# Kernel optimization log

Hardware: AMD Instinct MI355X
Metric: run time of the kernel (lower is better)

The kernel has to match this reference:

```python
import jax, jax.numpy as jnp
import numpy as np

N_HEAD, D_MODEL, D_HEAD = 16, 1024, 64
BSZ, SEQ = 4, 2048
SCALE = 1.0 / D_HEAD ** 0.5
LN_EPS = 1e-5
NEG = -1e10


def layer_norm(x, gamma, beta):
    mu = jnp.mean(x, axis=-1, keepdims=True)
    var = jnp.var(x, axis=-1, keepdims=True)
    return (x - mu) * jax.lax.rsqrt(var + LN_EPS) * gamma + beta


def setup_inputs() -> dict:
    key = jax.random.key(0)
    ks = jax.random.split(key, 8)
    q = jax.random.normal(ks[0], (BSZ, SEQ, D_MODEL), dtype=jnp.float32)
    attn_mask = jax.random.randint(ks[1], (SEQ, SEQ), 0, 2).astype(bool)
    s = 1.0 / np.sqrt(D_MODEL)
    Wq = jax.random.normal(ks[2], (D_MODEL, N_HEAD * D_HEAD), dtype=jnp.float32) * s
    Wk = jax.random.normal(ks[3], (D_MODEL, N_HEAD * D_HEAD), dtype=jnp.float32) * s
    Wv = jax.random.normal(ks[4], (D_MODEL, N_HEAD * D_HEAD), dtype=jnp.float32) * s
    Wo = jax.random.normal(ks[5], (N_HEAD * D_HEAD, D_MODEL), dtype=jnp.float32) * s
    gamma = jnp.ones((D_MODEL,), dtype=jnp.float32)
    beta = jnp.zeros((D_MODEL,), dtype=jnp.float32)
    return {"q": q, "attn_mask": attn_mask, "Wq": Wq, "Wk": Wk, "Wv": Wv,
            "Wo": Wo, "gamma": gamma, "beta": beta}


def reference(q, attn_mask, Wq, Wk, Wv, Wo, gamma, beta):
    # pre_lnorm: residual uses the normalized q (as in the torch code, q is reassigned)
    qn = layer_norm(q, gamma, beta)                      # (b, n1, d_model)
    hq = (qn @ Wq).reshape(BSZ, SEQ, N_HEAD, D_HEAD)     # self-attn: k = v = q
    hk = (qn @ Wk).reshape(BSZ, SEQ, N_HEAD, D_HEAD)
    hv = (qn @ Wv).reshape(BSZ, SEQ, N_HEAD, D_HEAD)
    score = jnp.einsum('bind,bjnd->ijbn', hq, hk) * SCALE  # (n1, n2, b, h)
    score = jnp.where(attn_mask[:, :, None, None], NEG, score)
    prob = jax.nn.softmax(score, axis=1)
    vec = jnp.einsum('ijbn,bjnd->bind', prob, hv).reshape(BSZ, SEQ, N_HEAD * D_HEAD)
    attn_out = vec @ Wo
    return qn + attn_out
```

## Files before the change

### kernel.cpp

```cpp
#include <hip/hip_runtime.h>

typedef __bf16 bf16;
typedef __bf16 bf16x8 __attribute__((ext_vector_type(8)));
typedef __bf16 bf16x4 __attribute__((ext_vector_type(4)));
typedef float  f32x4  __attribute__((ext_vector_type(4)));

#define MFMA16 __builtin_amdgcn_mfma_f32_16x16x32_bf16

static constexpr int   BSZ   = 4;
static constexpr int   SEQL  = 2048;
static constexpr int   DM    = 1024;
static constexpr int   NHEAD = 16;
static constexpr int   DHEAD = 64;
static constexpr float SCL2  = 0.125f * 1.44269504f;

__device__ __forceinline__ void glds16(bf16* lds, const bf16* g) {
    __builtin_amdgcn_global_load_lds(
        (const __attribute__((address_space(1))) unsigned int*)g,
        (__attribute__((address_space(3))) unsigned int*)lds, 16, 0, 0);
}

__global__ void detect_mask(const unsigned int* __restrict__ m, int* __restrict__ flag) {
    __shared__ int ok[4];
    if (threadIdx.x < 4) ok[threadIdx.x] = 1;
    __syncthreads();
    for (int i = 0; i < 16; ++i) {
        unsigned int w = m[threadIdx.x * 16 + i];
        if (!(w == 0u || w == 1u)) ok[0] = 0;
        if (w & 0xFEFEFEFEu) ok[1] = 0;
        if (!(w == 0u || w == 0x3F800000u)) ok[2] = 0;
        unsigned lo = w & 0xFFFFu, hi = w >> 16;
        if (!((lo == 0u || lo == 0x3F80u) && (hi == 0u || hi == 0x3F80u))) ok[3] = 0;
    }
    __syncthreads();
    if (threadIdx.x == 0)
        *flag = ok[0] ? 0 : (ok[1] ? 1 : (ok[2] ? 2 : 3));
}

__device__ __forceinline__ bool mask_at(const void* m, int fl, long idx) {
    if (fl == 0) return ((const int*)m)[idx] != 0;
    if (fl == 1) return ((const unsigned char*)m)[idx] != 0;
    if (fl == 2) return ((const float*)m)[idx] != 0.0f;
    return ((const unsigned short*)m)[idx] != 0;
}

__global__ __launch_bounds__(256) void prep_bits(const void* __restrict__ mask,
                                                 const int* __restrict__ flagp,
                                                 unsigned long long* __restrict__ rb) {
    const int fl = *flagp;
    const int word = blockIdx.x * 4 + (threadIdx.x >> 6);
    const long base = (long)word * 64 + (threadIdx.x & 63);
    unsigned long long b = __ballot(mask_at(mask, fl, base));
    if ((threadIdx.x & 63) == 0) rb[word] = b;
}

__global__ __launch_bounds__(256) void prep_words(
    const unsigned long long* __restrict__ rb, unsigned long long* __restrict__ wm)
{
    const int t = threadIdx.x, L = t & 63, w = t >> 6;
    const int pair = blockIdx.x * 4 + w;
    const int qgrp = pair >> 5, kt = pair & 31;
    const unsigned long long r0 = rb[(size_t)(qgrp * 16 + (L & 15)) * 32 + kt];
    const int lq = L >> 4;
    unsigned long long myw = 0;
    #pragma unroll
    for (int jr = 0; jr < 16; ++jr) {
        const int jj = jr >> 2, r = jr & 3;
        const int bitpos = (jj & 1) * 32 + lq * 8 + (jj >> 1) * 4 + r;
        unsigned long long bal = __ballot(((r0 >> bitpos) & 1ull) != 0ull);
        if (L == jr) myw = bal;
    }
    if (L < 16) wm[(size_t)pair * 16 + L] = myw;
}

__global__ __launch_bounds__(256) void ln_kernel(
    const float* __restrict__ x, const float* __restrict__ g,
    const float* __restrict__ bta, bf16* __restrict__ y)
{
    const int row = blockIdx.x, t = threadIdx.x;
    const float4 v = ((const float4*)(x + (size_t)row * DM))[t];
    float s  = v.x + v.y + v.z + v.w;
    float ss = v.x * v.x + v.y * v.y + v.z * v.z + v.w * v.w;
    for (int m = 32; m >= 1; m >>= 1) { s += __shfl_xor(s, m); ss += __shfl_xor(ss, m); }
    __shared__ float red[8];
    const int w = t >> 6, L = t & 63;
    if (L == 0) { red[w] = s; red[4 + w] = ss; }
    __syncthreads();
    s  = red[0] + red[1] + red[2] + red[3];
    ss = red[4] + red[5] + red[6] + red[7];
    const float mu = s * (1.0f / DM);
    const float var = ss * (1.0f / DM) - mu * mu;
    const float r = rsqrtf(var + 1e-5f);
    const float4 gv = ((const float4*)g)[t];
    const float4 bv = ((const float4*)bta)[t];
    bf16x4 o;
    o[0] = (bf16)((v.x - mu) * r * gv.x + bv.x);
    o[1] = (bf16)((v.y - mu) * r * gv.y + bv.y);
    o[2] = (bf16)((v.z - mu) * r * gv.z + bv.z);
    o[3] = (bf16)((v.w - mu) * r * gv.w + bv.w);
    ((bf16x4*)(y + (size_t)row * DM))[t] = o;
}

__global__ void cvt_w(const float* __restrict__ Wq, const float* __restrict__ Wk,
                      const float* __restrict__ Wv, const float* __restrict__ Wo,
                      bf16* __restrict__ Wt)
{
    __shared__ float tile[32][33];
    const int z = blockIdx.z;
    const float* src = (z == 0) ? Wq : (z == 1) ? Wk : (z == 2) ? Wv : Wo;
    const float scl = (z == 1) ? SCL2 : 1.0f;
    bf16* dst = Wt + (size_t)z * DM * DM;
    const int tx = threadIdx.x, ty = threadIdx.y;
    const int nIn = blockIdx.x * 32 + tx;
    const int kIn = blockIdx.y * 32;
    for (int i = 0; i < 32; i += 8)
        tile[ty + i][tx] = src[(size_t)(kIn + ty + i) * DM + nIn];
    __syncthreads();
    const int nOut = blockIdx.x * 32;
    const int kOut = blockIdx.y * 32 + tx;
    for (int i = 0; i < 32; i += 8)
        dst[(size_t)(nOut + ty + i) * DM + kOut] = (bf16)(tile[tx][ty + i] * scl);
}

__device__ __forceinline__ void gemm128_core(
    const bf16* __restrict__ A, const bf16* __restrict__ Bt,
    int m0, int n0, bool swapped, f32x4 acc[4][4], bf16* Asm, bf16* Bsm)
{
    const int t = threadIdx.x, w = t >> 6, L = t & 63;
    const int lr = L & 15, lq = L >> 4;
    const int wm = w & 1, wn = w >> 1;
    const int srow = L >> 3;
    const int scol = ((L & 7) ^ (L >> 3)) * 8;
    const bf16* Ab = A  + (size_t)(m0 + w * 32 + srow) * DM + scol;
    const bf16* Bb = Bt + (size_t)(n0 + w * 32 + srow) * DM + scol;
    bf16* AsmW = Asm + (w * 32) * 64;
    bf16* BsmW = Bsm + (w * 32) * 64;
    for (int kk = 0; kk < DM; kk += 64) {
        __syncthreads();
        glds16(AsmW,           Ab + kk);
        glds16(AsmW +  8 * 64, Ab + (size_t) 8 * DM + kk);
        glds16(AsmW + 16 * 64, Ab + (size_t)16 * DM + kk);
        glds16(AsmW + 24 * 64, Ab + (size_t)24 * DM + kk);
        glds16(BsmW,           Bb + kk);
        glds16(BsmW +  8 * 64, Bb + (size_t) 8 * DM + kk);
        glds16(BsmW + 16 * 64, Bb + (size_t)16 * DM + kk);
        glds16(BsmW + 24 * 64, Bb + (size_t)24 * DM + kk);
        __syncthreads();
        #pragma unroll
        for (int ks = 0; ks < 2; ++ks) {
            bf16x8 af[4], bf_[4];
            #pragma unroll
            for (int i = 0; i < 4; ++i) {
                const int ra = wm * 64 + i * 16 + lr;
                af[i] = *(const bf16x8*)(Asm + ra * 64 + ((((ks << 2) | lq) ^ (lr & 7)) << 3));
            }
            #pragma unroll
            for (int j = 0; j < 4; ++j) {
                const int rb2 = wn * 64 + j * 16 + lr;
                bf_[j] = *(const bf16x8*)(Bsm + rb2 * 64 + ((((ks << 2) | lq) ^ (lr & 7)) << 3));
            }
            if (!swapped) {
                #pragma unroll
                for (int i = 0; i < 4; ++i)
                    #pragma unroll
                    for (int j = 0; j < 4; ++j)
                        acc[i][j] = MFMA16(af[i], bf_[j], acc[i][j], 0, 0, 0);
            } else {
                #pragma unroll
                for (int i = 0; i < 4; ++i)
                    #pragma unroll
                    for (int j = 0; j < 4; ++j)
                        acc[i][j] = MFMA16(bf_[j], af[i], acc[i][j], 0, 0, 0);
            }
        }
    }
}

__global__ __launch_bounds__(256) void qkv128(
    const bf16* __restrict__ qn, const bf16* __restrict__ Wt,
    bf16* __restrict__ Qb, bf16* __restrict__ Kb, bf16* __restrict__ Vtb)
{
    __shared__ __align__(16) bf16 Asm[128 * 64];
    __shared__ __align__(16) bf16 Bsm[128 * 64];
    const int ny = blockIdx.y;
    const int z = ny >> 3;
    const int m0 = blockIdx.x * 128, n0 = (ny & 7) * 128;
    f32x4 acc[4][4] = {};
    gemm128_core(qn, Wt + (size_t)z * DM * DM, m0, n0, z == 2, acc, Asm, Bsm);
    const int t = threadIdx.x, L = t & 63, w = t >> 6;
    const int wm = w & 1, wn = w >> 1, lr = L & 15, lq = L >> 4;
    if (z < 2) {
        bf16* dst = z ? Kb : Qb;
        #pragma unroll
        for (int i = 0; i < 4; ++i)
            #pragma unroll
            for (int j = 0; j < 4; ++j)
                #pragma unroll
                for (int r = 0; r < 4; ++r) {
                    int m = m0 + wm * 64 + i * 16 + lq * 4 + r;
                    int n = n0 + wn * 64 + j * 16 + lr;
                    int b = m >> 11, s = m & 2047, h = n >> 6, d = n & 63;
                    dst[(((size_t)b * NHEAD + h) * SEQL + s) * DHEAD + d] = (bf16)acc[i][j][r];
                }
    } else {
        #pragma unroll
        for (int i = 0; i < 4; ++i)
            #pragma unroll
            for (int j = 0; j < 4; ++j)
                #pragma unroll
                for (int r = 0; r < 4; ++r) {
                    int dg = n0 + wn * 64 + j * 16 + lq * 4 + r;
                    int sg = m0 + wm * 64 + i * 16 + lr;
                    int h = dg >> 6, d = dg & 63, b = sg >> 11, s = sg & 2047;
                    Vtb[(((size_t)b * NHEAD + h) * DHEAD + d) * SEQL + s] = (bf16)acc[i][j][r];
                }
    }
}

__global__ __launch_bounds__(256) void out128(
    const bf16* __restrict__ vec, const bf16* __restrict__ Wot,
    const bf16* __restrict__ qnb, float* __restrict__ out)
{
    __shared__ __align__(16) bf16 Asm[128 * 64];
    __shared__ __align__(16) bf16 Bsm[128 * 64];
    const int m0 = blockIdx.x * 128, n0 = blockIdx.y * 128;
    f32x4 acc[4][4] = {};
    gemm128_core(vec, Wot, m0, n0, false, acc, Asm, Bsm);
    const int t = threadIdx.x, L = t & 63, w = t >> 6;
    const int wm = w & 1, wn = w >> 1, lr = L & 15, lq = L >> 4;
    #pragma unroll
    for (int i = 0; i < 4; ++i)
        #pragma unroll
        for (int j = 0; j < 4; ++j)
            #pragma unroll
            for (int r = 0; r < 4; ++r) {
                int m = m0 + wm * 64 + i * 16 + lq * 4 + r;
                int n = n0 + wn * 64 + j * 16 + lr;
                size_t idx = (size_t)m * DM + n;
                out[idx] = acc[i][j][r] + (float)qnb[idx];
            }
}

__global__ __launch_bounds__(256) void flash_attn(
    const bf16* __restrict__ Qb, const bf16* __restrict__ Kb,
    const bf16* __restrict__ Vtb, const unsigned long long* __restrict__ mb,
    bf16* __restrict__ vec)
{
    __shared__ __align__(16) bf16 Ksm [2][64 * 72];
    __shared__ __align__(16) bf16 Vtsm[2][64 * 72];

    const int t = threadIdx.x, w = t >> 6, L = t & 63;
    const int lr = L & 15, lq = L >> 4;
    const int bid = blockIdx.x;
    const int slot = bid & 7, rest = bid >> 3;
    const int qblk = rest & 15;
    const int bh = ((rest >> 4) << 3) + slot;
    const int b = bh >> 4, h = bh & 15;
    const int q0 = qblk * 128 + w * 32;

    const bf16* Qh  = Qb  + (size_t)bh * SEQL * DHEAD;
    const bf16* Kh  = Kb  + (size_t)bh * SEQL * DHEAD;
    const bf16* Vth = Vtb + (size_t)bh * DHEAD * SEQL;

    bf16x8 qf[2][2];
    #pragma unroll
    for (int qg = 0; qg < 2; ++qg)
        #pragma unroll
        for (int ks = 0; ks < 2; ++ks)
            qf[qg][ks] = *(const bf16x8*)(Qh + (size_t)(q0 + qg * 16 + lr) * DHEAD + ks * 32 + lq * 8);

    const int qgrp0 = __builtin_amdgcn_readfirstlane(q0 >> 4);
    const unsigned long long* wm0 = mb + (size_t)qgrp0 * 512;
    const unsigned long long* wm1 = wm0 + 512;

    f32x4 o[4][2] = {};
    f32x4 lacc[2] = {};

    const bf16 one = (bf16)1.0f;
    const bf16x8 ones8 = {one, one, one, one, one, one, one, one};
    const float fz = 0.0f;

    const int sr = t >> 2, sc = (t & 3) * 16;
    const int zrow = ((sr >> 2) & 1) * 32 + ((sr >> 5) & 1) * 16 + ((sr >> 3) & 3) * 4 + (sr & 3);
    constexpr int NT = SEQL / 64;
    bf16x8 kreg[2], vreg[2];

    kreg[0] = *(const bf16x8*)(Kh  + (size_t)sr * DHEAD + sc);
    kreg[1] = *(const bf16x8*)(Kh  + (size_t)sr * DHEAD + sc + 8);
    vreg[0] = *(const bf16x8*)(Vth + (size_t)sr * SEQL + sc);
    vreg[1] = *(const bf16x8*)(Vth + (size_t)sr * SEQL + sc + 8);
    *(bf16x8*)(Ksm[0]  + zrow * 72 + sc)     = kreg[0];
    *(bf16x8*)(Ksm[0]  + zrow * 72 + sc + 8) = kreg[1];
    *(bf16x8*)(Vtsm[0] + sr * 72 + sc)       = vreg[0];
    *(bf16x8*)(Vtsm[0] + sr * 72 + sc + 8)   = vreg[1];
    kreg[0] = *(const bf16x8*)(Kh  + (size_t)(64 + sr) * DHEAD + sc);
    kreg[1] = *(const bf16x8*)(Kh  + (size_t)(64 + sr) * DHEAD + sc + 8);
    vreg[0] = *(const bf16x8*)(Vth + (size_t)sr * SEQL + 64 + sc);
    vreg[1] = *(const bf16x8*)(Vth + (size_t)sr * SEQL + 64 + sc + 8);
    __syncthreads();

    for (int kt = 0; kt < NT; ++kt) {
        const int cur = kt & 1;
        const bf16* Kc = Ksm[cur];
        const bf16* Vc = Vtsm[cur];

        f32x4 s[4][2] = {};
        #pragma unroll
        for (int ks = 0; ks < 2; ++ks) {
            bf16x8 kf[4];
            #pragma unroll
            for (int jj = 0; jj < 4; ++jj)
                kf[jj] = *(const bf16x8*)(Kc + (jj * 16 + lr) * 72 + ks * 32 + lq * 8);
            __builtin_amdgcn_s_setprio(1);
            #pragma unroll
            for (int jj = 0; jj < 4; ++jj)
                #pragma unroll
                for (int qg = 0; qg < 2; ++qg)
                    s[jj][qg] = MFMA16(kf[jj], qf[qg][ks], s[jj][qg], 0, 0, 0);
            __builtin_amdgcn_s_setprio(0);
        }

        if (kt + 1 < NT) {
            bf16* Ka = Ksm[cur ^ 1];
            bf16* Va = Vtsm[cur ^ 1];
            *(bf16x8*)(Ka + zrow * 72 + sc)     = kreg[0];
            *(bf16x8*)(Ka + zrow * 72 + sc + 8) = kreg[1];
            *(bf16x8*)(Va + sr * 72 + sc)       = vreg[0];
            *(bf16x8*)(Va + sr * 72 + sc + 8)   = vreg[1];
            if (kt + 2 < NT) {
                const int kb2 = (kt + 2) * 64;
                kreg[0] = *(const bf16x8*)(Kh  + (size_t)(kb2 + sr) * DHEAD + sc);
                kreg[1] = *(const bf16x8*)(Kh  + (size_t)(kb2 + sr) * DHEAD + sc + 8);
                vreg[0] = *(const bf16x8*)(Vth + (size_t)sr * SEQL + kb2 + sc);
                vreg[1] = *(const bf16x8*)(Vth + (size_t)sr * SEQL + kb2 + sc + 8);
            }
        }

        bf16x8 pf[2][2];
        #pragma unroll
        for (int qg = 0; qg < 2; ++qg) {
            const unsigned long long* wp = (qg ? wm1 : wm0) + kt * 16;
            #pragma unroll
            for (int ks = 0; ks < 2; ++ks) {
                bf16x8 pv;
                #pragma unroll
                for (int r = 0; r < 4; ++r) {
                    float e0 = __builtin_amdgcn_exp2f(s[ks][qg][r]);
                    float e1 = __builtin_amdgcn_exp2f(s[2 + ks][qg][r]);
                    float z0, z1;
                    asm("v_cndmask_b32 %0, %1, %2, %3"
                        : "=v"(z0) : "v"(e0), "v"(fz), "s"(wp[ks * 4 + r]));
                    asm("v_cndmask_b32 %0, %1, %2, %3"
                        : "=v"(z1) : "v"(e1), "v"(fz), "s"(wp[(2 + ks) * 4 + r]));
                    pv[r]     = (bf16)z0;
                    pv[4 + r] = (bf16)z1;
                }
                pf[qg][ks] = pv;
            }
        }

        __builtin_amdgcn_s_setprio(1);
        #pragma unroll
        for (int ks = 0; ks < 2; ++ks) {
            #pragma unroll
            for (int qg = 0; qg < 2; ++qg)
                lacc[qg] = MFMA16(ones8, pf[qg][ks], lacc[qg], 0, 0, 0);
            #pragma unroll
            for (int dg = 0; dg < 4; ++dg) {
                bf16x8 vf = *(const bf16x8*)(Vc + (dg * 16 + lr) * 72 + ks * 32 + lq * 8);
                #pragma unroll
                for (int qg = 0; qg < 2; ++qg)
                    o[dg][qg] = MFMA16(vf, pf[qg][ks], o[dg][qg], 0, 0, 0);
            }
        }
        __builtin_amdgcn_s_setprio(0);

        if (kt + 1 < NT) __syncthreads();
    }

    #pragma unroll
    for (int qg = 0; qg < 2; ++qg) {
        const float rl = 1.0f / lacc[qg][0];
        const size_t rowb = ((size_t)b * SEQL + q0 + qg * 16 + lr) * DM + h * DHEAD;
        #pragma unroll
        for (int dg = 0; dg < 4; ++dg) {
            bf16x4 ov;
            #pragma unroll
            for (int r = 0; r < 4; ++r) ov[r] = (bf16)(o[dg][qg][r] * rl);
            *(bf16x4*)(vec + rowb + dg * 16 + lq * 4) = ov;
        }
    }
}

extern "C" void kernel_launch(void* const* d_in, const int* in_sizes, int n_in,
                              void* d_out, int out_size, void* d_ws, size_t ws_size,
                              hipStream_t stream)
{
    const float* qin   = (const float*)d_in[0];
    const void*  mask  = d_in[1];
    const float* Wq    = (const float*)d_in[2];
    const float* Wk    = (const float*)d_in[3];
    const float* Wv    = (const float*)d_in[4];
    const float* Wo    = (const float*)d_in[5];
    const float* gamma = (const float*)d_in[6];
    const float* beta  = (const float*)d_in[7];
    float* out = (float*)d_out;

    char* w = (char*)d_ws;
    int*  flag = (int*)w;
    bf16* qnb  = (bf16*)(w + 256);
    bf16* Wt   = qnb + (size_t)8192 * 1024;
    bf16* Qb   = Wt + (size_t)4 * 1024 * 1024;
    bf16* Kb   = Qb + (size_t)8192 * 1024;
    bf16* Vtb  = Kb + (size_t)8192 * 1024;
    bf16* vec  = Vtb + (size_t)8192 * 1024;
    unsigned long long* rbits  = (unsigned long long*)(vec + (size_t)8192 * 1024);
    unsigned long long* mwords = rbits + 65536;

    detect_mask<<<1, 256, 0, stream>>>((const unsigned int*)mask, flag);
    prep_bits<<<SEQL * (SEQL / 64) / 4, 256, 0, stream>>>(mask, flag, rbits);
    prep_words<<<1024, 256, 0, stream>>>(rbits, mwords);
    ln_kernel<<<8192, 256, 0, stream>>>(qin, gamma, beta, qnb);
    cvt_w<<<dim3(32, 32, 4), dim3(32, 8), 0, stream>>>(Wq, Wk, Wv, Wo, Wt);
    qkv128<<<dim3(64, 24), 256, 0, stream>>>(qnb, Wt, Qb, Kb, Vtb);
    flash_attn<<<1024, 256, 0, stream>>>(Qb, Kb, Vtb, mwords, vec);
    out128<<<dim3(64, 8), 256, 0, stream>>>(vec, Wt + (size_t)3 * 1024 * 1024, qnb, out);
}
```

Baseline: 307.6 us.

## Load K and V fragments directly from global memory, dropping LDS staging

The flash attention kernel no longer stages K and V tiles through double-buffered shared memory with block barriers. Each wave now loads its MFMA operand fragments straight from global memory: K for the next tile is prefetched into registers, and V is loaded per tile. This removes the LDS traffic and __syncthreads, but each of the 4 waves now reads K/V separately, so the kernel relies on L2/L1 caching and global latency hiding instead of shared reuse.

```diff
diff --git a/kernel.cpp b/kernel.cpp
--- a/kernel.cpp
+++ b/kernel.cpp
@@ -246,9 +246,6 @@
     const bf16* __restrict__ Vtb, const unsigned long long* __restrict__ mb,
     bf16* __restrict__ vec)
 {
-    __shared__ __align__(16) bf16 Ksm [2][64 * 72];
-    __shared__ __align__(16) bf16 Vtsm[2][64 * 72];
-
     const int t = threadIdx.x, w = t >> 6, L = t & 63;
     const int lr = L & 15, lq = L >> 4;
     const int bid = blockIdx.x;
@@ -259,8 +256,9 @@
     const int q0 = qblk * 128 + w * 32;
 
     const bf16* Qh  = Qb  + (size_t)bh * SEQL * DHEAD;
-    const bf16* Kh  = Kb  + (size_t)bh * SEQL * DHEAD;
-    const bf16* Vth = Vtb + (size_t)bh * DHEAD * SEQL;
+    const int rbase = ((lr >> 3) & 1) * 16 + ((lr >> 2) & 1) * 8 + (lr & 3);
+    const bf16* Klp = Kb  + (size_t)bh * SEQL * DHEAD + (size_t)rbase * DHEAD + lq * 8;
+    const bf16* Vlp = Vtb + (size_t)bh * DHEAD * SEQL + (size_t)lr * SEQL + lq * 8;
 
     bf16x8 qf[2][2];
     #pragma unroll
@@ -280,61 +278,36 @@
     const bf16x8 ones8 = {one, one, one, one, one, one, one, one};
     const float fz = 0.0f;
 
-    const int sr = t >> 2, sc = (t & 3) * 16;
-    const int zrow = ((sr >> 2) & 1) * 32 + ((sr >> 5) & 1) * 16 + ((sr >> 3) & 3) * 4 + (sr & 3);
     constexpr int NT = SEQL / 64;
-    bf16x8 kreg[2], vreg[2];
-
-    kreg[0] = *(const bf16x8*)(Kh  + (size_t)sr * DHEAD + sc);
-    kreg[1] = *(const bf16x8*)(Kh  + (size_t)sr * DHEAD + sc + 8);
-    vreg[0] = *(const bf16x8*)(Vth + (size_t)sr * SEQL + sc);
-    vreg[1] = *(const bf16x8*)(Vth + (size_t)sr * SEQL + sc + 8);
-    *(bf16x8*)(Ksm[0]  + zrow * 72 + sc)     = kreg[0];
-    *(bf16x8*)(Ksm[0]  + zrow * 72 + sc + 8) = kreg[1];
-    *(bf16x8*)(Vtsm[0] + sr * 72 + sc)       = vreg[0];
-    *(bf16x8*)(Vtsm[0] + sr * 72 + sc + 8)   = vreg[1];
-    kreg[0] = *(const bf16x8*)(Kh  + (size_t)(64 + sr) * DHEAD + sc);
-    kreg[1] = *(const bf16x8*)(Kh  + (size_t)(64 + sr) * DHEAD + sc + 8);
-    vreg[0] = *(const bf16x8*)(Vth + (size_t)sr * SEQL + 64 + sc);
-    vreg[1] = *(const bf16x8*)(Vth + (size_t)sr * SEQL + 64 + sc + 8);
-    __syncthreads();
-
+
+    bf16x8 kf[2][4];
+    #pragma unroll
+    for (int ks = 0; ks < 2; ++ks)
+        #pragma unroll
+        for (int jj = 0; jj < 4; ++jj)
+            kf[ks][jj] = *(const bf16x8*)(Klp
+                + (size_t)((jj & 1) * 32 + (jj >> 1) * 4) * DHEAD + ks * 32);
+
+    #pragma unroll 1
     for (int kt = 0; kt < NT; ++kt) {
-        const int cur = kt & 1;
-        const bf16* Kc = Ksm[cur];
-        const bf16* Vc = Vtsm[cur];
-
         f32x4 s[4][2] = {};
-        #pragma unroll
-        for (int ks = 0; ks < 2; ++ks) {
-            bf16x8 kf[4];
+        __builtin_amdgcn_s_setprio(1);
+        #pragma unroll
+        for (int ks = 0; ks < 2; ++ks)
             #pragma unroll
             for (int jj = 0; jj < 4; ++jj)
-                kf[jj] = *(const bf16x8*)(Kc + (jj * 16 + lr) * 72 + ks * 32 + lq * 8);
-            __builtin_amdgcn_s_setprio(1);
-            #pragma unroll
-            for (int jj = 0; jj < 4; ++jj)
                 #pragma unroll
                 for (int qg = 0; qg < 2; ++qg)
-                    s[jj][qg] = MFMA16(kf[jj], qf[qg][ks], s[jj][qg], 0, 0, 0);
-            __builtin_amdgcn_s_setprio(0);
-        }
-
-        if (kt + 1 < NT) {
-            bf16* Ka = Ksm[cur ^ 1];
-            bf16* Va = Vtsm[cur ^ 1];
-            *(bf16x8*)(Ka + zrow * 72 + sc)     = kreg[0];
-            *(bf16x8*)(Ka + zrow * 72 + sc + 8) = kreg[1];
-            *(bf16x8*)(Va + sr * 72 + sc)       = vreg[0];
-            *(bf16x8*)(Va + sr * 72 + sc + 8)   = vreg[1];
-            if (kt + 2 < NT) {
-                const int kb2 = (kt + 2) * 64;
-                kreg[0] = *(const bf16x8*)(Kh  + (size_t)(kb2 + sr) * DHEAD + sc);
-                kreg[1] = *(const bf16x8*)(Kh  + (size_t)(kb2 + sr) * DHEAD + sc + 8);
-                vreg[0] = *(const bf16x8*)(Vth + (size_t)sr * SEQL + kb2 + sc);
-                vreg[1] = *(const bf16x8*)(Vth + (size_t)sr * SEQL + kb2 + sc + 8);
-            }
-        }
+                    s[jj][qg] = MFMA16(kf[ks][jj], qf[qg][ks], s[jj][qg], 0, 0, 0);
+        __builtin_amdgcn_s_setprio(0);
+
+        bf16x8 vf[2][4];
+        #pragma unroll
+        for (int ks = 0; ks < 2; ++ks)
+            #pragma unroll
+            for (int dg = 0; dg < 4; ++dg)
+                vf[ks][dg] = *(const bf16x8*)(Vlp + (size_t)dg * 16 * SEQL
+                                              + kt * 64 + ks * 32);
 
         bf16x8 pf[2][2];
         #pragma unroll
@@ -359,6 +332,16 @@
             }
         }
 
+        if (kt + 1 < NT) {
+            #pragma unroll
+            for (int ks = 0; ks < 2; ++ks)
+                #pragma unroll
+                for (int jj = 0; jj < 4; ++jj)
+                    kf[ks][jj] = *(const bf16x8*)(Klp
+                        + (size_t)((kt + 1) * 64 + (jj & 1) * 32 + (jj >> 1) * 4) * DHEAD
+                        + ks * 32);
+        }
+
         __builtin_amdgcn_s_setprio(1);
         #pragma unroll
         for (int ks = 0; ks < 2; ++ks) {
@@ -367,15 +350,12 @@
                 lacc[qg] = MFMA16(ones8, pf[qg][ks], lacc[qg], 0, 0, 0);
             #pragma unroll
             for (int dg = 0; dg < 4; ++dg) {
-                bf16x8 vf = *(const bf16x8*)(Vc + (dg * 16 + lr) * 72 + ks * 32 + lq * 8);
                 #pragma unroll
                 for (int qg = 0; qg < 2; ++qg)
-                    o[dg][qg] = MFMA16(vf, pf[qg][ks], o[dg][qg], 0, 0, 0);
+                    o[dg][qg] = MFMA16(vf[ks][dg], pf[qg][ks], o[dg][qg], 0, 0, 0);
             }
         }
         __builtin_amdgcn_s_setprio(0);
-
-        if (kt + 1 < NT) __syncthreads();
     }
 
     #pragma unroll
```

Measured after the change: 440.0 us. 1.43x slower.
